# Kernel optimization log

Measured on AMD Instinct MI355X. Metric: run time of the kernel, lower is better.

## Reference

```python
import jax, jax.numpy as jnp
import numpy as np

B, T, N = 64, 100, 20000
ALPHA, BETA = 1.0, 0.5  # ExpRelu params


def setup_inputs() -> dict:
    rng = np.random.default_rng(0)
    # Proper SE(3) poses so the inverse is well-conditioned
    A = rng.normal(size=(B, 3, 3))
    Q, _ = np.linalg.qr(A)
    det = np.linalg.det(Q)
    Q[:, :, 0] *= det[:, None]  # force det(R) = +1
    poses = np.tile(np.eye(4, dtype=np.float64), (B, 1, 1))
    poses[:, :3, :3] = Q
    poses[:, :3, 3] = rng.normal(size=(B, 3)) * 10.0
    # Homogeneous global boundary points [4, N]
    pts = rng.normal(size=(3, N)) * 50.0
    boundary = np.concatenate([pts, np.ones((1, N))], axis=0)
    # Unit boundary normals [3, N]
    nrm = rng.normal(size=(3, N))
    nrm /= np.linalg.norm(nrm, axis=0, keepdims=True)
    # Local-frame waypoints [B, T, 3]
    wpts = rng.normal(size=(B, T, 3)) * 5.0
    return {
        "posesglobal": jnp.asarray(poses, dtype=jnp.float32),
        "waypointslocal": jnp.asarray(wpts, dtype=jnp.float32),
        "boundary": jnp.asarray(boundary, dtype=jnp.float32),
        "boundarynormals": jnp.asarray(nrm, dtype=jnp.float32),
    }


def _exp_relu(x):
    return jnp.where(x > 0.0, ALPHA * x + 1.0, jnp.exp(BETA * x))


def reference(posesglobal, waypointslocal, boundary, boundarynormals):
    posesinv = jnp.linalg.inv(posesglobal)                     # [B,4,4]
    # boundary points into each local frame: [B,N,3]
    bpl = jnp.einsum("bij,jn->bni", posesinv, boundary)[..., :3]
    # rotate normals into local frame: [B,N,3]
    bnl = jnp.einsum("bij,jn->bni", posesinv[:, :3, :3], boundarynormals)
    # 1-NN search: squared distances [B,T,N] (argmin-equivalent to cdist)
    w2 = jnp.sum(waypointslocal * waypointslocal, axis=-1)     # [B,T]
    p2 = jnp.sum(bpl * bpl, axis=-1)                           # [B,N]
    cross = jnp.einsum("btd,bnd->btn", waypointslocal, bpl)    # [B,T,N]
    d2 = w2[:, :, None] + p2[:, None, :] - 2.0 * cross
    idx = jnp.argmin(d2, axis=2)                               # [B,T]
    cp = jnp.take_along_axis(bpl, idx[..., None], axis=1)      # [B,T,3]
    cn = jnp.take_along_axis(bnl, idx[..., None], axis=1)      # [B,T,3]
    dots = jnp.sum((waypointslocal - cp) * cn, axis=2)         # [B,T]
    loss = jnp.mean(jnp.mean(_exp_relu(dots), axis=1))         # scalar
    return loss
```

## Files before the change

kernel.cpp:

```cpp
#include <hip/hip_runtime.h>
#include <math.h>
#include <float.h>

#define B_ 64
#define T_ 100
#define N_ 20000
#define NQ (B_ * T_)
#define NCHUNKS 100
#define CHUNK (N_ / NCHUNKS)
#define PAIRS (CHUNK / 2)
#define GROUPS (PAIRS / 2)
#define QG 256
#define NQG (NQ / QG)
#define K1_THREADS 128

typedef float f2 __attribute__((ext_vector_type(2)));
typedef float f4 __attribute__((ext_vector_type(4)));
typedef unsigned long long u64;

#define KEYS_OFF 0

__device__ __forceinline__ unsigned int f32_sortable(float f) {
    unsigned int u = __float_as_uint(f);
    return ((int)u >= 0) ? (u | 0x80000000u) : ~u;
}

__global__ __launch_bounds__(256) void k0_init(u64* __restrict__ keys,
                                               float* __restrict__ out)
{
    const int i = blockIdx.x * 256 + threadIdx.x;
    keys[i] = ~0ull;
    if (i == 0) out[0] = 0.0f;
}

__global__ __launch_bounds__(K1_THREADS) void k1_nn(
    const float* __restrict__ poses,
    const float* __restrict__ wpts,
    const float* __restrict__ boundary,
    u64* __restrict__ keys)
{
    __shared__ f4 sh[PAIRS][2];
    const int bx   = blockIdx.x;
    const int qg   = bx / NCHUNKS;
    const int c    = bx - qg * NCHUNKS;
    const int base = c * CHUNK;
    const int tid  = threadIdx.x;

    if (tid < PAIRS) {
        const int p  = tid;
        const int n0 = base + 2 * p;
        const float x0 = boundary[n0],          x1 = boundary[n0 + 1];
        const float y0 = boundary[N_ + n0],     y1 = boundary[N_ + n0 + 1];
        const float z0 = boundary[2 * N_ + n0], z1 = boundary[2 * N_ + n0 + 1];
        f4 a = { -2.f * x0, -2.f * x1, -2.f * y0, -2.f * y1 };
        f4 b = { -2.f * z0, -2.f * z1,
                 x0 * x0 + y0 * y0 + z0 * z0,
                 x1 * x1 + y1 * y1 + z1 * z1 };
        sh[p][0] = a;
        sh[p][1] = b;
    }

    const int i0 = qg * QG + tid;
    const int i1 = i0 + K1_THREADS;

    float q0x, q0y, q0z, q1x, q1y, q1z;
    {
        int b0 = i0 / T_;
        const float* P = poses + b0 * 16;
        const float* W = wpts + i0 * 3;
        float wx = W[0], wy = W[1], wz = W[2];
        q0x = P[0] * wx + P[1] * wy + P[2]  * wz + P[3];
        q0y = P[4] * wx + P[5] * wy + P[6]  * wz + P[7];
        q0z = P[8] * wx + P[9] * wy + P[10] * wz + P[11];
    }
    {
        int b1 = i1 / T_;
        const float* P = poses + b1 * 16;
        const float* W = wpts + i1 * 3;
        float wx = W[0], wy = W[1], wz = W[2];
        q1x = P[0] * wx + P[1] * wy + P[2]  * wz + P[3];
        q1y = P[4] * wx + P[5] * wy + P[6]  * wz + P[7];
        q1z = P[8] * wx + P[9] * wy + P[10] * wz + P[11];
    }
    __syncthreads();

    const f2 v0x = { q0x, q0x }, v0y = { q0y, q0y }, v0z = { q0z, q0z };
    const f2 v1x = { q1x, q1x }, v1y = { q1y, q1y }, v1z = { q1z, q1z };

    float best0 = FLT_MAX, best1 = FLT_MAX;
    int   bg0 = 0, bg1 = 0;

#pragma unroll 5
    for (int g = 0; g < GROUPS; ++g) {
        const f4 a0 = sh[2 * g][0],     b0 = sh[2 * g][1];
        const f4 a1 = sh[2 * g + 1][0], b1 = sh[2 * g + 1][1];
        const f2 mx0 = { a0.x, a0.y }, my0 = { a0.z, a0.w };
        const f2 mz0 = { b0.x, b0.y }, p20 = { b0.z, b0.w };
        const f2 mx1 = { a1.x, a1.y }, my1 = { a1.z, a1.w };
        const f2 mz1 = { b1.x, b1.y }, p21 = { b1.z, b1.w };

        f2 eA = __builtin_elementwise_fma(mx0, v0x,
                __builtin_elementwise_fma(my0, v0y,
                __builtin_elementwise_fma(mz0, v0z, p20)));
        f2 eB = __builtin_elementwise_fma(mx1, v0x,
                __builtin_elementwise_fma(my1, v0y,
                __builtin_elementwise_fma(mz1, v0z, p21)));
        float m0 = fminf(fminf(eA.x, eA.y), fminf(eB.x, eB.y));
        if (m0 < best0) { best0 = m0; bg0 = g; }

        f2 eC = __builtin_elementwise_fma(mx0, v1x,
                __builtin_elementwise_fma(my0, v1y,
                __builtin_elementwise_fma(mz0, v1z, p20)));
        f2 eD = __builtin_elementwise_fma(mx1, v1x,
                __builtin_elementwise_fma(my1, v1y,
                __builtin_elementwise_fma(mz1, v1z, p21)));
        float m1 = fminf(fminf(eC.x, eC.y), fminf(eD.x, eD.y));
        if (m1 < best1) { best1 = m1; bg1 = g; }
    }

    {
        const f4 a0 = sh[2 * bg0][0],     b0 = sh[2 * bg0][1];
        const f4 a1 = sh[2 * bg0 + 1][0], b1 = sh[2 * bg0 + 1][1];
        const f2 mx0 = { a0.x, a0.y }, my0 = { a0.z, a0.w };
        const f2 mz0 = { b0.x, b0.y }, p20 = { b0.z, b0.w };
        const f2 mx1 = { a1.x, a1.y }, my1 = { a1.z, a1.w };
        const f2 mz1 = { b1.x, b1.y }, p21 = { b1.z, b1.w };
        f2 eA = __builtin_elementwise_fma(mx0, v0x,
                __builtin_elementwise_fma(my0, v0y,
                __builtin_elementwise_fma(mz0, v0z, p20)));
        f2 eB = __builtin_elementwise_fma(mx1, v0x,
                __builtin_elementwise_fma(my1, v0y,
                __builtin_elementwise_fma(mz1, v0z, p21)));
        int loc = 4 * bg0;
        int li = (eA.x == best0) ? loc
               : (eA.y == best0) ? loc + 1
               : (eB.x == best0) ? loc + 2 : loc + 3;
        u64 key = ((u64)f32_sortable(best0) << 32) | (unsigned)(base + li);
        atomicMin(&keys[i0], key);
    }
    {
        const f4 a0 = sh[2 * bg1][0],     b0 = sh[2 * bg1][1];
        const f4 a1 = sh[2 * bg1 + 1][0], b1 = sh[2 * bg1 + 1][1];
        const f2 mx0 = { a0.x, a0.y }, my0 = { a0.z, a0.w };
        const f2 mz0 = { b0.x, b0.y }, p20 = { b0.z, b0.w };
        const f2 mx1 = { a1.x, a1.y }, my1 = { a1.z, a1.w };
        const f2 mz1 = { b1.x, b1.y }, p21 = { b1.z, b1.w };
        f2 eC = __builtin_elementwise_fma(mx0, v1x,
                __builtin_elementwise_fma(my0, v1y,
                __builtin_elementwise_fma(mz0, v1z, p20)));
        f2 eD = __builtin_elementwise_fma(mx1, v1x,
                __builtin_elementwise_fma(my1, v1y,
                __builtin_elementwise_fma(mz1, v1z, p21)));
        int loc = 4 * bg1;
        int li = (eC.x == best1) ? loc
               : (eC.y == best1) ? loc + 1
               : (eD.x == best1) ? loc + 2 : loc + 3;
        u64 key = ((u64)f32_sortable(best1) << 32) | (unsigned)(base + li);
        atomicMin(&keys[i1], key);
    }
}

__global__ __launch_bounds__(256) void k2_epilogue(
    const float* __restrict__ poses,
    const float* __restrict__ wpts,
    const float* __restrict__ boundary,
    const float* __restrict__ bnorm,
    const u64* __restrict__ keys,
    float* __restrict__ out)
{
    const int tid = threadIdx.x;
    const int i = blockIdx.x * 256 + tid;

    const int bi = (int)(unsigned)(keys[i] & 0xFFFFFFFFull);

    const int b = i / T_;
    const float* P = poses + b * 16;
    const float* W = wpts + i * 3;
    const float wx = W[0], wy = W[1], wz = W[2];
    const float qx = P[0] * wx + P[1] * wy + P[2]  * wz + P[3];
    const float qy = P[4] * wx + P[5] * wy + P[6]  * wz + P[7];
    const float qz = P[8] * wx + P[9] * wy + P[10] * wz + P[11];

    const float gx = boundary[bi], gy = boundary[N_ + bi], gz = boundary[2 * N_ + bi];
    const float nx = bnorm[bi],    ny = bnorm[N_ + bi],    nz = bnorm[2 * N_ + bi];

    const float dots = (qx - gx) * nx + (qy - gy) * ny + (qz - gz) * nz;
    float val = (dots > 0.0f) ? (dots + 1.0f) : expf(0.5f * dots);
    val *= (1.0f / (float)NQ);

    __shared__ float red[256];
    red[tid] = val;
    __syncthreads();
#pragma unroll
    for (int s = 128; s > 0; s >>= 1) {
        if (tid < s) red[tid] += red[tid + s];
        __syncthreads();
    }
    if (tid == 0) atomicAdd(out, red[0]);
}

extern "C" void kernel_launch(void* const* d_in, const int* in_sizes, int n_in,
                              void* d_out, int out_size, void* d_ws, size_t ws_size,
                              hipStream_t stream) {
    const float* poses    = (const float*)d_in[0];
    const float* wpts     = (const float*)d_in[1];
    const float* boundary = (const float*)d_in[2];
    const float* bnorm    = (const float*)d_in[3];
    float* out = (float*)d_out;

    u64* keys = (u64*)((char*)d_ws + KEYS_OFF);

    k0_init<<<NQ / 256, 256, 0, stream>>>(keys, out);
    k1_nn<<<NQG * NCHUNKS, K1_THREADS, 0, stream>>>(
        poses, wpts, boundary, keys);
    k2_epilogue<<<NQ / 256, 256, 0, stream>>>(
        poses, wpts, boundary, bnorm, keys, out);
}
```

Before: 81.05 us.

## Precompute boundary layout globally and stream it with wave-uniform scalar loads in NN search

A prep kernel now writes the transformed boundary data (-2x, -2y, -2z, |p|^2) to workspace once. The keys and output initialisation are folded into that same kernel. The NN kernel maps 64 queries to the lanes of each wave, and each wave scans its own slice of the boundary with wave-uniform addresses, which the compiler can serve through scalar loads. This removes the per-block LDS staging and __syncthreads, but the inner loop now depends on scalar-cache and L2 bandwidth, each lane holds one query instead of two, and 20 slices per query still race on atomicMin.

```diff
diff --git a/kernel.cpp b/kernel.cpp
--- a/kernel.cpp
+++ b/kernel.cpp
@@ -6,49 +6,41 @@
 #define T_ 100
 #define N_ 20000
 #define NQ (B_ * T_)
-#define NCHUNKS 100
-#define CHUNK (N_ / NCHUNKS)
-#define PAIRS (CHUNK / 2)
-#define GROUPS (PAIRS / 2)
-#define QG 256
-#define NQG (NQ / QG)
-#define K1_THREADS 128
+#define NP2 (N_ / 2)
+#define NG8 (N_ / 8)
+#define NSL 5
+#define WPB 4
+#define GPW (NG8 / (NSL * WPB))
 
 typedef float f2 __attribute__((ext_vector_type(2)));
 typedef float f4 __attribute__((ext_vector_type(4)));
 typedef unsigned long long u64;
 
 #define KEYS_OFF 0
+#define PREP_OFF (NQ * 8)
 
 __device__ __forceinline__ unsigned int f32_sortable(float f) {
     unsigned int u = __float_as_uint(f);
     return ((int)u >= 0) ? (u | 0x80000000u) : ~u;
 }
 
-__global__ __launch_bounds__(256) void k0_init(u64* __restrict__ keys,
-                                               float* __restrict__ out)
-{
-    const int i = blockIdx.x * 256 + threadIdx.x;
-    keys[i] = ~0ull;
-    if (i == 0) out[0] = 0.0f;
+__device__ __forceinline__ f2 edist2(f4 A, f4 Bv, f2 vx, f2 vy, f2 vz) {
+    f2 mx = { A.x,  A.y  }, my = { A.z,  A.w  };
+    f2 mz = { Bv.x, Bv.y }, p2 = { Bv.z, Bv.w };
+    return __builtin_elementwise_fma(mx, vx,
+           __builtin_elementwise_fma(my, vy,
+           __builtin_elementwise_fma(mz, vz, p2)));
 }
 
-__global__ __launch_bounds__(K1_THREADS) void k1_nn(
-    const float* __restrict__ poses,
-    const float* __restrict__ wpts,
+__global__ __launch_bounds__(256) void k_prep(
     const float* __restrict__ boundary,
-    u64* __restrict__ keys)
+    f4* __restrict__ prep,
+    u64* __restrict__ keys,
+    float* __restrict__ out)
 {
-    __shared__ f4 sh[PAIRS][2];
-    const int bx   = blockIdx.x;
-    const int qg   = bx / NCHUNKS;
-    const int c    = bx - qg * NCHUNKS;
-    const int base = c * CHUNK;
-    const int tid  = threadIdx.x;
-
-    if (tid < PAIRS) {
-        const int p  = tid;
-        const int n0 = base + 2 * p;
+    const int t = blockIdx.x * 256 + threadIdx.x;
+    if (t < NP2) {
+        const int n0 = 2 * t;
         const float x0 = boundary[n0],          x1 = boundary[n0 + 1];
         const float y0 = boundary[N_ + n0],     y1 = boundary[N_ + n0 + 1];
         const float z0 = boundary[2 * N_ + n0], z1 = boundary[2 * N_ + n0 + 1];
@@ -56,111 +48,79 @@
         f4 b = { -2.f * z0, -2.f * z1,
                  x0 * x0 + y0 * y0 + z0 * z0,
                  x1 * x1 + y1 * y1 + z1 * z1 };
-        sh[p][0] = a;
-        sh[p][1] = b;
+        prep[2 * t]     = a;
+        prep[2 * t + 1] = b;
     }
+    if (t < NQ) keys[t] = ~0ull;
+    if (t == 0) out[0] = 0.0f;
+}
 
-    const int i0 = qg * QG + tid;
-    const int i1 = i0 + K1_THREADS;
+__global__ __launch_bounds__(256) void k_nn(
+    const float* __restrict__ poses,
+    const float* __restrict__ wpts,
+    const f4* __restrict__ prep,
+    u64* __restrict__ keys)
+{
+    const int qg   = blockIdx.x / NSL;
+    const int sl   = blockIdx.x - qg * NSL;
+    const int lane = threadIdx.x & 63;
+    const int wv   = __builtin_amdgcn_readfirstlane((int)(threadIdx.x >> 6));
 
-    float q0x, q0y, q0z, q1x, q1y, q1z;
-    {
-        int b0 = i0 / T_;
-        const float* P = poses + b0 * 16;
-        const float* W = wpts + i0 * 3;
-        float wx = W[0], wy = W[1], wz = W[2];
-        q0x = P[0] * wx + P[1] * wy + P[2]  * wz + P[3];
-        q0y = P[4] * wx + P[5] * wy + P[6]  * wz + P[7];
-        q0z = P[8] * wx + P[9] * wy + P[10] * wz + P[11];
-    }
-    {
-        int b1 = i1 / T_;
-        const float* P = poses + b1 * 16;
-        const float* W = wpts + i1 * 3;
-        float wx = W[0], wy = W[1], wz = W[2];
-        q1x = P[0] * wx + P[1] * wy + P[2]  * wz + P[3];
-        q1y = P[4] * wx + P[5] * wy + P[6]  * wz + P[7];
-        q1z = P[8] * wx + P[9] * wy + P[10] * wz + P[11];
-    }
-    __syncthreads();
+    const int i = qg * 64 + lane;
+    const int b = i / T_;
+    const float* P = poses + b * 16;
+    const float* W = wpts + i * 3;
+    const float wx = W[0], wy = W[1], wz = W[2];
+    const float qx = P[0] * wx + P[1] * wy + P[2]  * wz + P[3];
+    const float qy = P[4] * wx + P[5] * wy + P[6]  * wz + P[7];
+    const float qz = P[8] * wx + P[9] * wy + P[10] * wz + P[11];
+    const f2 vx = { qx, qx }, vy = { qy, qy }, vz = { qz, qz };
 
-    const f2 v0x = { q0x, q0x }, v0y = { q0y, q0y }, v0z = { q0z, q0z };
-    const f2 v1x = { q1x, q1x }, v1y = { q1y, q1y }, v1z = { q1z, q1z };
+    const int g0 = (sl * WPB + wv) * GPW;
 
-    float best0 = FLT_MAX, best1 = FLT_MAX;
-    int   bg0 = 0, bg1 = 0;
+    float best = FLT_MAX;
+    int   bg   = g0;
 
 #pragma unroll 5
-    for (int g = 0; g < GROUPS; ++g) {
-        const f4 a0 = sh[2 * g][0],     b0 = sh[2 * g][1];
-        const f4 a1 = sh[2 * g + 1][0], b1 = sh[2 * g + 1][1];
-        const f2 mx0 = { a0.x, a0.y }, my0 = { a0.z, a0.w };
-        const f2 mz0 = { b0.x, b0.y }, p20 = { b0.z, b0.w };
-        const f2 mx1 = { a1.x, a1.y }, my1 = { a1.z, a1.w };
-        const f2 mz1 = { b1.x, b1.y }, p21 = { b1.z, b1.w };
+    for (int g = g0; g < g0 + GPW; ++g) {
+        const f4* p8 = prep + 8 * g;
+        const f4 A0 = p8[0], B0 = p8[1], A1 = p8[2], B1 = p8[3];
+        const f4 A2 = p8[4], B2 = p8[5], A3 = p8[6], B3 = p8[7];
 
-        f2 eA = __builtin_elementwise_fma(mx0, v0x,
-                __builtin_elementwise_fma(my0, v0y,
-                __builtin_elementwise_fma(mz0, v0z, p20)));
-        f2 eB = __builtin_elementwise_fma(mx1, v0x,
-                __builtin_elementwise_fma(my1, v0y,
-                __builtin_elementwise_fma(mz1, v0z, p21)));
-        float m0 = fminf(fminf(eA.x, eA.y), fminf(eB.x, eB.y));
-        if (m0 < best0) { best0 = m0; bg0 = g; }
+        const f2 e0 = edist2(A0, B0, vx, vy, vz);
+        const f2 e1 = edist2(A1, B1, vx, vy, vz);
+        const f2 e2 = edist2(A2, B2, vx, vy, vz);
+        const f2 e3 = edist2(A3, B3, vx, vy, vz);
 
-        f2 eC = __builtin_elementwise_fma(mx0, v1x,
-                __builtin_elementwise_fma(my0, v1y,
-                __builtin_elementwise_fma(mz0, v1z, p20)));
-        f2 eD = __builtin_elementwise_fma(mx1, v1x,
-                __builtin_elementwise_fma(my1, v1y,
-                __builtin_elementwise_fma(mz1, v1z, p21)));
-        float m1 = fminf(fminf(eC.x, eC.y), fminf(eD.x, eD.y));
-        if (m1 < best1) { best1 = m1; bg1 = g; }
+        const f2 m01 = __builtin_elementwise_min(e0, e1);
+        const f2 m23 = __builtin_elementwise_min(e2, e3);
+        const f2 m   = __builtin_elementwise_min(m01, m23);
+        const float s = fminf(m.x, m.y);
+        if (s < best) { best = s; bg = g; }
     }
 
     {
-        const f4 a0 = sh[2 * bg0][0],     b0 = sh[2 * bg0][1];
-        const f4 a1 = sh[2 * bg0 + 1][0], b1 = sh[2 * bg0 + 1][1];
-        const f2 mx0 = { a0.x, a0.y }, my0 = { a0.z, a0.w };
-        const f2 mz0 = { b0.x, b0.y }, p20 = { b0.z, b0.w };
-        const f2 mx1 = { a1.x, a1.y }, my1 = { a1.z, a1.w };
-        const f2 mz1 = { b1.x, b1.y }, p21 = { b1.z, b1.w };
-        f2 eA = __builtin_elementwise_fma(mx0, v0x,
-                __builtin_elementwise_fma(my0, v0y,
-                __builtin_elementwise_fma(mz0, v0z, p20)));
-        f2 eB = __builtin_elementwise_fma(mx1, v0x,
-                __builtin_elementwise_fma(my1, v0y,
-                __builtin_elementwise_fma(mz1, v0z, p21)));
-        int loc = 4 * bg0;
-        int li = (eA.x == best0) ? loc
-               : (eA.y == best0) ? loc + 1
-               : (eB.x == best0) ? loc + 2 : loc + 3;
-        u64 key = ((u64)f32_sortable(best0) << 32) | (unsigned)(base + li);
-        atomicMin(&keys[i0], key);
-    }
-    {
-        const f4 a0 = sh[2 * bg1][0],     b0 = sh[2 * bg1][1];
-        const f4 a1 = sh[2 * bg1 + 1][0], b1 = sh[2 * bg1 + 1][1];
-        const f2 mx0 = { a0.x, a0.y }, my0 = { a0.z, a0.w };
-        const f2 mz0 = { b0.x, b0.y }, p20 = { b0.z, b0.w };
-        const f2 mx1 = { a1.x, a1.y }, my1 = { a1.z, a1.w };
-        const f2 mz1 = { b1.x, b1.y }, p21 = { b1.z, b1.w };
-        f2 eC = __builtin_elementwise_fma(mx0, v1x,
-                __builtin_elementwise_fma(my0, v1y,
-                __builtin_elementwise_fma(mz0, v1z, p20)));
-        f2 eD = __builtin_elementwise_fma(mx1, v1x,
-                __builtin_elementwise_fma(my1, v1y,
-                __builtin_elementwise_fma(mz1, v1z, p21)));
-        int loc = 4 * bg1;
-        int li = (eC.x == best1) ? loc
-               : (eC.y == best1) ? loc + 1
-               : (eD.x == best1) ? loc + 2 : loc + 3;
-        u64 key = ((u64)f32_sortable(best1) << 32) | (unsigned)(base + li);
-        atomicMin(&keys[i1], key);
+        const f4* p8 = prep + 8 * bg;
+        const f4 A0 = p8[0], B0 = p8[1], A1 = p8[2], B1 = p8[3];
+        const f4 A2 = p8[4], B2 = p8[5], A3 = p8[6], B3 = p8[7];
+        const f2 e0 = edist2(A0, B0, vx, vy, vz);
+        const f2 e1 = edist2(A1, B1, vx, vy, vz);
+        const f2 e2 = edist2(A2, B2, vx, vy, vz);
+        const f2 e3 = edist2(A3, B3, vx, vy, vz);
+        const int loc = 8 * bg;
+        int li = (e0.x == best) ? loc
+               : (e0.y == best) ? loc + 1
+               : (e1.x == best) ? loc + 2
+               : (e1.y == best) ? loc + 3
+               : (e2.x == best) ? loc + 4
+               : (e2.y == best) ? loc + 5
+               : (e3.x == best) ? loc + 6 : loc + 7;
+        u64 key = ((u64)f32_sortable(best) << 32) | (unsigned)li;
+        atomicMin(&keys[i], key);
     }
 }
 
-__global__ __launch_bounds__(256) void k2_epilogue(
+__global__ __launch_bounds__(256) void k_epilogue(
     const float* __restrict__ poses,
     const float* __restrict__ wpts,
     const float* __restrict__ boundary,
@@ -209,10 +169,10 @@
     float* out = (float*)d_out;
 
     u64* keys = (u64*)((char*)d_ws + KEYS_OFF);
+    f4*  prep = (f4*)((char*)d_ws + PREP_OFF);
 
-    k0_init<<<NQ / 256, 256, 0, stream>>>(keys, out);
-    k1_nn<<<NQG * NCHUNKS, K1_THREADS, 0, stream>>>(
-        poses, wpts, boundary, keys);
-    k2_epilogue<<<NQ / 256, 256, 0, stream>>>(
+    k_prep<<<40, 256, 0, stream>>>(boundary, prep, keys, out);
+    k_nn<<<100 * NSL, 256, 0, stream>>>(poses, wpts, prep, keys);
+    k_epilogue<<<NQ / 256, 256, 0, stream>>>(
         poses, wpts, boundary, bnorm, keys, out);
 }
```

After: 97.50 us. 1.2x slower.
